# Kernel tuning notes

Measured on AMD Instinct MI355X. Metric: run time of the kernel, lower is better.

The kernel has to match this reference:

```python
import jax, jax.numpy as jnp
import numpy as np

N_NODES = 100000
N_EDGES = 3200000


def _spmm(rows, cols, vals, x):
    # out[i] = sum_{e: rows[e]==i} vals[e] * x[cols[e]]
    msgs = vals[:, None] * x[cols]  # [E, F]
    return jax.ops.segment_sum(msgs, rows, num_segments=N_NODES)


def setup_inputs() -> dict:
    key = jax.random.key(0)
    ks = jax.random.split(key, 8)
    x = jax.random.normal(ks[0], (N_NODES, 256), dtype=jnp.float32)
    adj_rows = jax.random.randint(ks[1], (N_EDGES,), 0, N_NODES, dtype=jnp.int32)
    adj_cols = jax.random.randint(ks[2], (N_EDGES,), 0, N_NODES, dtype=jnp.int32)
    adj_vals = jax.random.uniform(ks[3], (N_EDGES,), dtype=jnp.float32)
    W1 = jax.random.normal(ks[4], (256, 128), dtype=jnp.float32) * (1.0 / np.sqrt(256))
    b1 = jnp.zeros((128,), dtype=jnp.float32)
    W2 = jax.random.normal(ks[5], (128, 64), dtype=jnp.float32) * (1.0 / np.sqrt(128))
    b2 = jnp.zeros((64,), dtype=jnp.float32)
    return {"x": x, "adj_rows": adj_rows, "adj_cols": adj_cols, "adj_vals": adj_vals,
            "W1": W1, "b1": b1, "W2": W2, "b2": b2}


def reference(x, adj_rows, adj_cols, adj_vals, W1, b1, W2, b2):
    # Layer 0: spmm -> linear -> relu (dropout inactive in eval)
    h = _spmm(adj_rows, adj_cols, adj_vals, x)
    h = jax.nn.relu(h @ W1 + b1)
    # Layer 1 (last layer): spmm -> linear, no activation
    h = _spmm(adj_rows, adj_cols, adj_vals, h)
    out = h @ W2 + b2
    return out  # squeeze(1) is a no-op for [N, nclass]
```

## Files before the change

### kernel.cpp

```cpp
#include <hip/hip_runtime.h>
#include <hip/hip_fp16.h>


#define PCHUNK 8192
#define EPT 32
#define ROWCAP 96

typedef _Float16 half8 __attribute__((ext_vector_type(8)));
typedef _Float16 h2t __attribute__((ext_vector_type(2)));
typedef float floatx4 __attribute__((ext_vector_type(4)));

__global__ __launch_bounds__(256) void prep_weights_kernel(const float* __restrict__ W1,
                                                           const float* __restrict__ W2,
                                                           __half* __restrict__ W1T,
                                                           h2t* __restrict__ pk,
                                                           int* __restrict__ cnt, int nN) {
    int i = blockIdx.x * 256 + threadIdx.x;
    if (i < 256 * 128) {
        int k = i >> 7, n = i & 127;
        W1T[n * 256 + k] = __float2half_rn(W1[i]);
    } else if (i < 256 * 128 + 4096) {
        int j = i - 256 * 128;
        int kk = j >> 6, c = j & 63;
        h2t v;
        v[0] = (_Float16)W2[(2 * kk) * 64 + c];
        v[1] = (_Float16)W2[(2 * kk + 1) * 64 + c];
        pk[j] = v;
    } else {
        int j = i - (256 * 128 + 4096);
        if (j < nN) cnt[j] = 0;
    }
}

__global__ __launch_bounds__(256) void transpose_w_kernel(const float* __restrict__ W,
                                                          __half* __restrict__ WT,
                                                          int K, int N) {
    int i = blockIdx.x * 256 + threadIdx.x;
    if (i < K * N) {
        int k = i / N, n = i % N;
        WT[n * K + k] = __float2half_rn(W[i]);
    }
}

__global__ __launch_bounds__(256) void gemm_scatter_kernel(
    const float* __restrict__ A, const __half* __restrict__ BT,
    __half* __restrict__ C, int nrows,
    const int* __restrict__ rows, const int* __restrict__ cols,
    const float* __restrict__ vals, int* __restrict__ cnt,
    int2* __restrict__ eb2, int nE, int scblocks) {
    extern __shared__ char smem[];
    const int t = threadIdx.x;

    if ((int)blockIdx.x < scblocks) {
        const int c0 = blockIdx.x * PCHUNK;
#pragma unroll 4
        for (int j = 0; j < EPT; ++j) {
            int e = c0 + t + 256 * j;
            if (e < nE) {
                int r = rows[e];
                int slot = atomicAdd(&cnt[r], 1);
                if (slot < ROWCAP)
                    eb2[(size_t)r * ROWCAP + slot] =
                        make_int2(cols[e], __float_as_int(vals[e]));
            }
        }
    } else {
        constexpr int MT = 64, KT = 32, KP = KT + 8, NN = 128, KK = 256;
        constexpr int WCT = NN / 32;
        __half* As = (__half*)smem;
        __half* Bs = As + MT * KP;
        const int wid = t >> 6, lane = t & 63;
        const int row0 = ((int)blockIdx.x - scblocks) * MT;
        const int wr = wid & 1, wc = wid >> 1;
        const int lrow = lane & 15, q = lane >> 4;

        floatx4 acc[2][WCT];
#pragma unroll
        for (int rt = 0; rt < 2; ++rt)
#pragma unroll
            for (int ct = 0; ct < WCT; ++ct)
#pragma unroll
                for (int i = 0; i < 4; ++i) acc[rt][ct][i] = 0.f;

        for (int kt = 0; kt < KK; kt += KT) {
#pragma unroll
            for (int it = 0; it < MT * KT / 4 / 256; ++it) {
                int i4 = it * 256 + t;
                int m = i4 >> 3;
                int kk = (i4 & 7) << 2;
                int gr = row0 + m;
                float4 v = make_float4(0.f, 0.f, 0.f, 0.f);
                if (gr < nrows) v = *(const float4*)(A + (size_t)gr * KK + kt + kk);
                __half h0 = __float2half_rn(v.x), h1 = __float2half_rn(v.y);
                __half h2 = __float2half_rn(v.z), h3 = __float2half_rn(v.w);
                ushort4 u = make_ushort4(*(unsigned short*)&h0, *(unsigned short*)&h1,
                                         *(unsigned short*)&h2, *(unsigned short*)&h3);
                *(ushort4*)(As + m * KP + kk) = u;
            }
#pragma unroll
            for (int it = 0; it < NN * KT / 4 / 256; ++it) {
                int i4 = it * 256 + t;
                int n = i4 >> 3;
                int kk = (i4 & 7) << 2;
                *(ushort4*)(Bs + n * KP + kk) =
                    *(const ushort4*)(BT + (size_t)n * KK + kt + kk);
            }
            __syncthreads();

            half8 a0 = *(half8*)(As + (wr * 32 + lrow) * KP + q * 8);
            half8 a1 = *(half8*)(As + (wr * 32 + 16 + lrow) * KP + q * 8);
#pragma unroll
            for (int ct = 0; ct < WCT; ++ct) {
                half8 b = *(half8*)(Bs + (wc * (NN / 2) + ct * 16 + lrow) * KP + q * 8);
                acc[0][ct] = __builtin_amdgcn_mfma_f32_16x16x32_f16(a0, b, acc[0][ct], 0, 0, 0);
                acc[1][ct] = __builtin_amdgcn_mfma_f32_16x16x32_f16(a1, b, acc[1][ct], 0, 0, 0);
            }
            __syncthreads();
        }

#pragma unroll
        for (int rt = 0; rt < 2; ++rt)
#pragma unroll
            for (int ct = 0; ct < WCT; ++ct)
#pragma unroll
                for (int r = 0; r < 4; ++r) {
                    int gr = row0 + wr * 32 + rt * 16 + q * 4 + r;
                    if (gr < nrows)
                        C[(size_t)gr * NN + wc * (NN / 2) + ct * 16 + lrow] =
                            __float2half_rn(acc[rt][ct][r]);
                }
    }
}

__global__ __launch_bounds__(256) void spmm_fused_kernel(const int* __restrict__ cnt,
                                                         const int2* __restrict__ eb,
                                                         const __half* __restrict__ Y,
                                                         const float* __restrict__ b1,
                                                         const h2t* __restrict__ pk,
                                                         __half* __restrict__ Y2, int nN) {
    __shared__ h2t w2s[64 * 64];
    __shared__ h2t hs[4][64];
    const int t = threadIdx.x;
#pragma unroll
    for (int i = 0; i < 16; ++i) w2s[i * 256 + t] = pk[i * 256 + t];
    __syncthreads();

    const int wv = t >> 6;
    const int lane = t & 63;
    const int fg = lane & 15;
    const int g = lane >> 4;
    const int gw = blockIdx.x * 4 + wv;
    const int nw = gridDim.x * 4;

    for (int row = gw; row < nN; row += nw) {
        float acc[8];
#pragma unroll
        for (int p = 0; p < 8; ++p) acc[p] = 0.f;

        int len = cnt[row];
        if (len > ROWCAP) len = ROWCAP;
        int s = row * ROWCAP;
        int e1 = s + len;
        for (int base = s; base < e1; base += 64) {
            int n = min(64, e1 - base);
            int2 my = (lane < n) ? eb[base + lane] : make_int2(0, 0);
            for (int j = 0; j < n; j += 8) {
                int i0 = j + g;
                int i1 = j + 4 + g;
                int s0 = (i0 < n) ? i0 : j;
                int s1 = (i1 < n) ? i1 : j;
                int c0 = __shfl(my.x, s0);
                int c1 = __shfl(my.x, s1);
                float v0 = __int_as_float(__shfl(my.y, s0));
                float v1 = __int_as_float(__shfl(my.y, s1));
                if (i0 >= n) v0 = 0.f;
                if (i1 >= n) v1 = 0.f;
                half8 y0 = *(const half8*)(Y + ((size_t)c0 << 7) + (fg << 3));
                half8 y1 = *(const half8*)(Y + ((size_t)c1 << 7) + (fg << 3));
#pragma unroll
                for (int p = 0; p < 8; ++p) acc[p] = fmaf(v0, (float)y0[p], acc[p]);
#pragma unroll
                for (int p = 0; p < 8; ++p) acc[p] = fmaf(v1, (float)y1[p], acc[p]);
            }
        }
#pragma unroll
        for (int p = 0; p < 8; ++p) acc[p] += __shfl_xor(acc[p], 16);
#pragma unroll
        for (int p = 0; p < 8; ++p) acc[p] += __shfl_xor(acc[p], 32);

        if (g == 0) {
            floatx4 ba = *(const floatx4*)(b1 + fg * 8);
            floatx4 bb = *(const floatx4*)(b1 + fg * 8 + 4);
            float f[8];
#pragma unroll
            for (int p = 0; p < 4; ++p) f[p] = fmaxf(acc[p] + ba[p], 0.f);
#pragma unroll
            for (int p = 0; p < 4; ++p) f[4 + p] = fmaxf(acc[4 + p] + bb[p], 0.f);
#pragma unroll
            for (int p = 0; p < 4; ++p) {
                h2t pr;
                pr[0] = (_Float16)f[2 * p];
                pr[1] = (_Float16)f[2 * p + 1];
                hs[wv][fg * 4 + p] = pr;
            }
        }
        __builtin_amdgcn_sched_barrier(0);

        float o = 0.f;
#pragma unroll 8
        for (int kk = 0; kk < 64; ++kk) {
            h2t a = hs[wv][kk];
            h2t b = w2s[kk * 64 + lane];
#if __has_builtin(__builtin_amdgcn_fdot2)
            o = __builtin_amdgcn_fdot2(a, b, o, false);
#else
            o = fmaf((float)a[0], (float)b[0], o);
            o = fmaf((float)a[1], (float)b[1], o);
#endif
        }
        Y2[(size_t)row * 64 + lane] = __float2half_rn(o);
    }
}

__global__ __launch_bounds__(256) void spmm_csr64_kernel(const int* __restrict__ cnt,
                                                         const int2* __restrict__ eb,
                                                         const __half* __restrict__ Y,
                                                         const float* __restrict__ bias,
                                                         float* __restrict__ out, int nN) {
    const int lane = threadIdx.x & 63;
    const int fg = lane & 7;
    const int g = lane >> 3;
    const int gw = blockIdx.x * 4 + (threadIdx.x >> 6);
    const int nw = gridDim.x * 4;

    for (int row = gw; row < nN; row += nw) {
        float acc[8];
#pragma unroll
        for (int p = 0; p < 8; ++p) acc[p] = 0.f;

        int len = cnt[row];
        if (len > ROWCAP) len = ROWCAP;
        int s = row * ROWCAP;
        int e1 = s + len;
        for (int base = s; base < e1; base += 64) {
            int n = min(64, e1 - base);
            int2 my = (lane < n) ? eb[base + lane] : make_int2(0, 0);
            for (int j = 0; j < n; j += 16) {
                int i0 = j + g;
                int i1 = j + 8 + g;
                int s0 = (i0 < n) ? i0 : j;
                int s1 = (i1 < n) ? i1 : j;
                int c0 = __shfl(my.x, s0);
                int c1 = __shfl(my.x, s1);
                float v0 = __int_as_float(__shfl(my.y, s0));
                float v1 = __int_as_float(__shfl(my.y, s1));
                if (i0 >= n) v0 = 0.f;
                if (i1 >= n) v1 = 0.f;
                half8 y0 = *(const half8*)(Y + ((size_t)c0 << 6) + (fg << 3));
                half8 y1 = *(const half8*)(Y + ((size_t)c1 << 6) + (fg << 3));
#pragma unroll
                for (int p = 0; p < 8; ++p) acc[p] = fmaf(v0, (float)y0[p], acc[p]);
#pragma unroll
                for (int p = 0; p < 8; ++p) acc[p] = fmaf(v1, (float)y1[p], acc[p]);
            }
        }
#pragma unroll
        for (int p = 0; p < 8; ++p) acc[p] += __shfl_xor(acc[p], 8);
#pragma unroll
        for (int p = 0; p < 8; ++p) acc[p] += __shfl_xor(acc[p], 16);
#pragma unroll
        for (int p = 0; p < 8; ++p) acc[p] += __shfl_xor(acc[p], 32);

        if (g == 0) {
            floatx4 ba = *(const floatx4*)(bias + fg * 8);
            floatx4 bb = *(const floatx4*)(bias + fg * 8 + 4);
            floatx4 o0, o1;
#pragma unroll
            for (int p = 0; p < 4; ++p) o0[p] = acc[p] + ba[p];
#pragma unroll
            for (int p = 0; p < 4; ++p) o1[p] = acc[4 + p] + bb[p];
            float* op = out + (size_t)row * 64 + fg * 8;
            *(floatx4*)op = o0;
            *(floatx4*)(op + 4) = o1;
        }
    }
}

__global__ __launch_bounds__(256) void init_bias_kernel(float* __restrict__ out,
                                                        const float* __restrict__ bias,
                                                        int fmask, size_t total) {
    size_t i = (size_t)blockIdx.x * 256 + threadIdx.x;
    if (i < total) out[i] = bias[i & fmask];
}

template <int F>
__global__ __launch_bounds__(256) void spmm_atomic_kernel(const int* __restrict__ rows,
                                                          const int* __restrict__ cols,
                                                          const float* __restrict__ vals,
                                                          const __half* __restrict__ Y,
                                                          float* __restrict__ out, int nE) {
    int e = blockIdx.x * 4 + (threadIdx.x >> 6);
    if (e >= nE) return;
    int lane = threadIdx.x & 63;
    int r = rows[e];
    int c = cols[e];
    float v = vals[e];
    if (F == 128) {
        float2 y = __half22float2(*((const __half2*)(Y + (size_t)c * 128) + lane));
        float* op = out + (size_t)r * 128 + lane * 2;
        unsafeAtomicAdd(op, v * y.x);
        unsafeAtomicAdd(op + 1, v * y.y);
    } else {
        float y = __half2float(Y[(size_t)c * F + lane]);
        unsafeAtomicAdd(out + (size_t)r * F + lane, v * y);
    }
}

template <int NN, int KK, bool RELU_IN>
__global__ __launch_bounds__(256) void gemm_mfma_kernel(const float* __restrict__ A,
                                                        const __half* __restrict__ BT,
                                                        __half* __restrict__ C, int nrows) {
    constexpr int MT = 64, KT = 64, KP = KT + 8;
    __shared__ __half As[MT * KP];
    __shared__ __half Bs[NN * KP];
    const int tid = threadIdx.x;
    const int wid = tid >> 6, lane = tid & 63;
    const int row0 = blockIdx.x * MT;
    const int wr = wid & 1, wc = wid >> 1;
    constexpr int WCT = NN / 32;
    const int lrow = lane & 15, q = lane >> 4;

    floatx4 acc[2][WCT];
#pragma unroll
    for (int rt = 0; rt < 2; ++rt)
#pragma unroll
        for (int ct = 0; ct < WCT; ++ct)
#pragma unroll
            for (int i = 0; i < 4; ++i) acc[rt][ct][i] = 0.f;

    for (int kt = 0; kt < KK; kt += KT) {
#pragma unroll
        for (int it = 0; it < MT * KT / 4 / 256; ++it) {
            int i4 = it * 256 + tid;
            int m = i4 >> 4;
            int kk = (i4 & 15) << 2;
            int gr = row0 + m;
            float4 v = make_float4(0.f, 0.f, 0.f, 0.f);
            if (gr < nrows) v = *(const float4*)(A + (size_t)gr * KK + kt + kk);
            if (RELU_IN) {
                v.x = fmaxf(v.x, 0.f); v.y = fmaxf(v.y, 0.f);
                v.z = fmaxf(v.z, 0.f); v.w = fmaxf(v.w, 0.f);
            }
            __half h0 = __float2half_rn(v.x), h1 = __float2half_rn(v.y);
            __half h2 = __float2half_rn(v.z), h3 = __float2half_rn(v.w);
            ushort4 u = make_ushort4(*(unsigned short*)&h0, *(unsigned short*)&h1,
                                     *(unsigned short*)&h2, *(unsigned short*)&h3);
            *(ushort4*)(As + m * KP + kk) = u;
        }
#pragma unroll
        for (int it = 0; it < NN * KT / 4 / 256; ++it) {
            int i4 = it * 256 + tid;
            int n = i4 >> 4;
            int kk = (i4 & 15) << 2;
            *(ushort4*)(Bs + n * KP + kk) =
                *(const ushort4*)(BT + (size_t)n * KK + kt + kk);
        }
        __syncthreads();

#pragma unroll
        for (int ks = 0; ks < KT; ks += 32) {
            half8 a0 = *(half8*)(As + (wr * 32 + lrow) * KP + ks + q * 8);
            half8 a1 = *(half8*)(As + (wr * 32 + 16 + lrow) * KP + ks + q * 8);
#pragma unroll
            for (int ct = 0; ct < WCT; ++ct) {
                half8 b = *(half8*)(Bs + (wc * (NN / 2) + ct * 16 + lrow) * KP + ks + q * 8);
                acc[0][ct] = __builtin_amdgcn_mfma_f32_16x16x32_f16(a0, b, acc[0][ct], 0, 0, 0);
                acc[1][ct] = __builtin_amdgcn_mfma_f32_16x16x32_f16(a1, b, acc[1][ct], 0, 0, 0);
            }
        }
        __syncthreads();
    }

#pragma unroll
    for (int rt = 0; rt < 2; ++rt)
#pragma unroll
        for (int ct = 0; ct < WCT; ++ct)
#pragma unroll
            for (int r = 0; r < 4; ++r) {
                int gr = row0 + wr * 32 + rt * 16 + q * 4 + r;
                if (gr < nrows)
                    C[(size_t)gr * NN + wc * (NN / 2) + ct * 16 + lrow] =
                        __float2half_rn(acc[rt][ct][r]);
            }
}

extern "C" void kernel_launch(void* const* d_in, const int* in_sizes, int n_in,
                              void* d_out, int out_size, void* d_ws, size_t ws_size,
                              hipStream_t stream) {
    const float* x    = (const float*)d_in[0];
    const int*   rows = (const int*)d_in[1];
    const int*   cols = (const int*)d_in[2];
    const float* vals = (const float*)d_in[3];
    const float* W1   = (const float*)d_in[4];
    const float* b1   = (const float*)d_in[5];
    const float* W2   = (const float*)d_in[6];
    const float* b2   = (const float*)d_in[7];
    float* out = (float*)d_out;

    const int nN = in_sizes[0] / 256;
    const int nE = in_sizes[1];

    const int mblocks  = (nN + 63) / 64;
    const int scblocks = (nE + PCHUNK - 1) / PCHUNK;
    const int sblocks  = min(2048, (nN + 3) / 4);
    const int eblocks4 = (nE + 3) / 4;

    char* w = (char*)d_ws;
    __half* Y1h = (__half*)w;  w += (size_t)nN * 128 * 2;
    __half* Y2h = (__half*)w;  w += (size_t)nN * 64 * 2;
    __half* W1T = (__half*)w;  w += (size_t)256 * 128 * 2;
    h2t*    pk  = (h2t*)w;     w += (size_t)4096 * 4;
    int*    cnt = (int*)w;     w += (size_t)nN * 4;
    int2*   eb2 = (int2*)w;    w += (size_t)nN * ROWCAP * 8;
    size_t need = (size_t)(w - (char*)d_ws);

    if (ws_size >= need && nN <= (1 << 17)) {
        prep_weights_kernel<<<(256 * 128 + 4096 + nN + 255) / 256, 256, 0, stream>>>(
            W1, W2, W1T, pk, cnt, nN);

        gemm_scatter_kernel<<<scblocks + mblocks, 256, (64 + 128) * 40 * 2, stream>>>(
            x, W1T, Y1h, nN, rows, cols, vals, cnt, eb2, nE, scblocks);

        spmm_fused_kernel<<<sblocks, 256, 0, stream>>>(cnt, eb2, Y1h, b1, pk, Y2h, nN);
        spmm_csr64_kernel<<<sblocks, 256, 0, stream>>>(cnt, eb2, Y2h, b2, out, nN);
    } else {
        char* v = (char*)d_ws;
        __half* fY1h = (__half*)v;  v += (size_t)nN * 128 * 2;
        float*  fH1  = (float*)v;   v += (size_t)nN * 128 * 4;
        __half* fW1T = (__half*)v;  v += (size_t)256 * 128 * 2;
        __half* fW2T = (__half*)v;  v += (size_t)128 * 64 * 2;

        transpose_w_kernel<<<(256 * 128 + 255) / 256, 256, 0, stream>>>(W1, fW1T, 256, 128);
        transpose_w_kernel<<<(128 * 64 + 255) / 256, 256, 0, stream>>>(W2, fW2T, 128, 64);
        gemm_mfma_kernel<128, 256, false><<<mblocks, 256, 0, stream>>>(x, fW1T, fY1h, nN);
        size_t totH1 = (size_t)nN * 128;
        init_bias_kernel<<<(int)((totH1 + 255) / 256), 256, 0, stream>>>(fH1, b1, 127, totH1);
        spmm_atomic_kernel<128><<<eblocks4, 256, 0, stream>>>(rows, cols, vals, fY1h, fH1, nE);
        gemm_mfma_kernel<64, 128, true><<<mblocks, 256, 0, stream>>>(fH1, fW2T, fY1h, nN);
        size_t totOut = (size_t)nN * 64;
        init_bias_kernel<<<(int)((totOut + 255) / 256), 256, 0, stream>>>(out, b2, 63, totOut);
        spmm_atomic_kernel<64><<<eblocks4, 256, 0, stream>>>(rows, cols, vals, fY1h, out, nE);
    }
}
```

Baseline: 493.0 us.

## Partition edge scatter by XCD row range with persistent work-queue blocks

Replaces the one-block-per-chunk scatter/GEMM launch with a persistent kernel of 2048 blocks. Blocks pull chunks from atomic work queues, and each XCD (read via the XCC_ID hardware register) scatters only edges whose destination row falls in its own slice of rows. The goal is to keep atomics and bucket writes local to each XCD's L2 and to reduce cross-die traffic. Each XCD now reads the full edge list, so edge reads grow eightfold, and ROWCAP drops from 96 to 72 to shrink the bucket buffer, guarded by an average-degree check. The GEMM tiles are also fetched from a queue after the scatter loop finishes.

```diff
diff --git a/kernel.cpp b/kernel.cpp
--- a/kernel.cpp
+++ b/kernel.cpp
@@ -4,7 +4,8 @@
 
 #define PCHUNK 8192
 #define EPT 32
-#define ROWCAP 96
+#define ROWCAP 72
+#define NXCD 8
 
 typedef _Float16 half8 __attribute__((ext_vector_type(8)));
 typedef _Float16 h2t __attribute__((ext_vector_type(2)));
@@ -14,7 +15,8 @@
                                                            const float* __restrict__ W2,
                                                            __half* __restrict__ W1T,
                                                            h2t* __restrict__ pk,
-                                                           int* __restrict__ cnt, int nN) {
+                                                           int* __restrict__ cnt, int nN,
+                                                           int* __restrict__ wq) {
     int i = blockIdx.x * 256 + threadIdx.x;
     if (i < 256 * 128) {
         int k = i >> 7, n = i & 127;
@@ -26,8 +28,10 @@
         v[0] = (_Float16)W2[(2 * kk) * 64 + c];
         v[1] = (_Float16)W2[(2 * kk + 1) * 64 + c];
         pk[j] = v;
+    } else if (i < 256 * 128 + 4096 + 129) {
+        wq[i - (256 * 128 + 4096)] = 0;
     } else {
-        int j = i - (256 * 128 + 4096);
+        int j = i - (256 * 128 + 4096 + 129);
         if (j < nN) cnt[j] = 0;
     }
 }
@@ -42,37 +46,62 @@
     }
 }
 
-__global__ __launch_bounds__(256) void gemm_scatter_kernel(
+__global__ __launch_bounds__(256) void gemm_scatter2_kernel(
     const float* __restrict__ A, const __half* __restrict__ BT,
     __half* __restrict__ C, int nrows,
     const int* __restrict__ rows, const int* __restrict__ cols,
     const float* __restrict__ vals, int* __restrict__ cnt,
-    int2* __restrict__ eb2, int nE, int scblocks) {
+    int2* __restrict__ eb2, int nE, int nN,
+    int* __restrict__ wq, int nchunks, int mblocks) {
     extern __shared__ char smem[];
+    __shared__ int sck;
     const int t = threadIdx.x;
-
-    if ((int)blockIdx.x < scblocks) {
-        const int c0 = blockIdx.x * PCHUNK;
+    const int rpx = (nN + NXCD - 1) / NXCD;
+
+    unsigned xcc;
+    asm volatile("s_getreg_b32 %0, hwreg(HW_REG_XCC_ID)" : "=s"(xcc));
+    const int my_xcd = (int)(xcc & (NXCD - 1));
+    const int rlo = my_xcd * rpx;
+    const int rhi = rlo + rpx;
+
+    for (;;) {
+        if (t == 0) sck = atomicAdd(&wq[my_xcd * 16], 1);
+        __syncthreads();
+        int ck = sck;
+        if (ck >= nchunks) break;
+        const int c0 = ck * PCHUNK;
 #pragma unroll 4
         for (int j = 0; j < EPT; ++j) {
             int e = c0 + t + 256 * j;
             if (e < nE) {
                 int r = rows[e];
-                int slot = atomicAdd(&cnt[r], 1);
-                if (slot < ROWCAP)
-                    eb2[(size_t)r * ROWCAP + slot] =
-                        make_int2(cols[e], __float_as_int(vals[e]));
-            }
-        }
-    } else {
-        constexpr int MT = 64, KT = 32, KP = KT + 8, NN = 128, KK = 256;
-        constexpr int WCT = NN / 32;
-        __half* As = (__half*)smem;
-        __half* Bs = As + MT * KP;
-        const int wid = t >> 6, lane = t & 63;
-        const int row0 = ((int)blockIdx.x - scblocks) * MT;
-        const int wr = wid & 1, wc = wid >> 1;
-        const int lrow = lane & 15, q = lane >> 4;
+                if (r >= rlo && r < rhi) {
+                    int c = cols[e];
+                    float v = vals[e];
+                    int slot = atomicAdd(&cnt[r], 1);
+                    if (slot < ROWCAP)
+                        eb2[(size_t)r * ROWCAP + slot] = make_int2(c, __float_as_int(v));
+                }
+            }
+        }
+        __syncthreads();
+    }
+    __syncthreads();
+
+    constexpr int MT = 64, KT = 32, KP = KT + 8, NN = 128, KK = 256;
+    constexpr int WCT = NN / 32;
+    __half* As = (__half*)smem;
+    __half* Bs = As + MT * KP;
+    const int wid = t >> 6, lane = t & 63;
+    const int wr = wid & 1, wc = wid >> 1;
+    const int lrow = lane & 15, q = lane >> 4;
+
+    for (;;) {
+        if (t == 0) sck = atomicAdd(&wq[128], 1);
+        __syncthreads();
+        int tl = sck;
+        if (tl >= mblocks) break;
+        const int row0 = tl * MT;
 
         floatx4 acc[2][WCT];
 #pragma unroll
@@ -411,7 +440,7 @@
     const int nE = in_sizes[1];
 
     const int mblocks  = (nN + 63) / 64;
-    const int scblocks = (nE + PCHUNK - 1) / PCHUNK;
+    const int nchunks  = (nE + PCHUNK - 1) / PCHUNK;
     const int sblocks  = min(2048, (nN + 3) / 4);
     const int eblocks4 = (nE + 3) / 4;
 
@@ -421,15 +450,18 @@
     __half* W1T = (__half*)w;  w += (size_t)256 * 128 * 2;
     h2t*    pk  = (h2t*)w;     w += (size_t)4096 * 4;
     int*    cnt = (int*)w;     w += (size_t)nN * 4;
+    int*    wq  = (int*)w;     w += (size_t)129 * 4;
     int2*   eb2 = (int2*)w;    w += (size_t)nN * ROWCAP * 8;
     size_t need = (size_t)(w - (char*)d_ws);
 
-    if (ws_size >= need && nN <= (1 << 17)) {
-        prep_weights_kernel<<<(256 * 128 + 4096 + nN + 255) / 256, 256, 0, stream>>>(
-            W1, W2, W1T, pk, cnt, nN);
-
-        gemm_scatter_kernel<<<scblocks + mblocks, 256, (64 + 128) * 40 * 2, stream>>>(
-            x, W1T, Y1h, nN, rows, cols, vals, cnt, eb2, nE, scblocks);
+    const bool cap_ok = (nE / nN) <= 36;
+
+    if (ws_size >= need && nN <= (1 << 17) && cap_ok) {
+        prep_weights_kernel<<<(256 * 128 + 4096 + 129 + nN + 255) / 256, 256, 0, stream>>>(
+            W1, W2, W1T, pk, cnt, nN, wq);
+
+        gemm_scatter2_kernel<<<2048, 256, (64 + 128) * 40 * 2, stream>>>(
+            x, W1T, Y1h, nN, rows, cols, vals, cnt, eb2, nE, nN, wq, nchunks, mblocks);
 
         spmm_fused_kernel<<<sblocks, 256, 0, stream>>>(cnt, eb2, Y1h, b1, pk, Y2h, nN);
         spmm_csr64_kernel<<<sblocks, 256, 0, stream>>>(cnt, eb2, Y2h, b2, out, nN);
```

New measurement: 612.4 us. +24.2%, slower.
